# Kernel tuning notes

Hardware: AMD Instinct MI355X
Metric: run time of the kernel (lower is better)

## Reference

```python
import jax, jax.numpy as jnp
import numpy as np

B, S, E, H = 4, 2048, 256, 8
D = E // H
SCALE = D ** -0.5


def setup_inputs() -> dict:
    key = jax.random.key(0)
    k1, k2, k3, k4, k5, k6 = jax.random.split(key, 6)
    x = jax.random.normal(k1, (B, S, E), dtype=jnp.float32)
    lengths = jax.random.randint(k2, (B,), S // 4, S + 1)
    # binary prefix mask, as assumed by mask[i].sum() == valid length in the original
    mask = (jnp.arange(S)[None, :] < lengths[:, None]).astype(jnp.int32)
    w_std = 1.0 / np.sqrt(E)
    Wq = jax.random.normal(k3, (E, E), dtype=jnp.float32) * w_std
    Wk = jax.random.normal(k4, (E, E), dtype=jnp.float32) * w_std
    Wv = jax.random.normal(k5, (E, E), dtype=jnp.float32) * w_std
    Wo = jax.random.normal(k6, (E, E), dtype=jnp.float32) * w_std
    return {"x": x, "mask": mask, "Wq": Wq, "Wk": Wk, "Wv": Wv, "Wo": Wo}


def _scramble_pad(attn_i, L):
    # attn_i: [S, H, D] attention output for one sample; only query rows < L are used.
    # Faithful to torch: attn[:L] viewed as [H, L, D] (after transpose(1,2)) then
    # reshape(L, E), zero-padded to [S, E]. The reshape mixes heads in a
    # length-dependent way, reproduced here with integer index arithmetic.
    L_safe = jnp.maximum(L, 1)
    flat = jnp.arange(S * E)                     # flat index into [H, L, D] row-major
    h = jnp.minimum(flat // (L_safe * D), H - 1)
    rem = flat % (L_safe * D)
    s = rem // D
    d = rem % D
    valid = flat < L * E
    vals = attn_i[s, h, d]
    return jnp.where(valid, vals, 0.0).reshape(S, E)


def reference(x, mask, Wq, Wk, Wv, Wo):
    # projections (torch Linear, no bias: y = x @ W.T), split heads
    Q = (x @ Wq.T).reshape(B, S, H, D)
    K = (x @ Wk.T).reshape(B, S, H, D)
    V = (x @ Wv.T).reshape(B, S, H, D)
    scores = jnp.einsum("bqhd,bkhd->bhqk", Q, K) * SCALE
    key_valid = mask[:, None, None, :] > 0       # prefix key mask == per-sample varlen attn
    scores = jnp.where(key_valid, scores, -1e30)
    P = jax.nn.softmax(scores, axis=-1)
    attn = jnp.einsum("bhqk,bkhd->bqhd", P, V)   # [B, S, H, D]
    lengths = mask.sum(axis=1)
    padded = jax.vmap(_scramble_pad)(attn, lengths)  # [B, S, E]
    return padded @ Wo.T
```

## Files before the change

kernel.cpp:

```cpp
#include <hip/hip_runtime.h>
#include <cmath>

#define Bn 4
#define Sn 2048
#define En 256
#define Hn 8
#define Dn 32
#define KD 256
#define NS 4
#define CHUNK 512

static constexpr float SCALE_F = 0.17677669529663687f;
static constexpr float SCALE_LOG2E = 0.25504210472155044f;

typedef _Float16 half4_t __attribute__((ext_vector_type(4)));
typedef _Float16 half8_t __attribute__((ext_vector_type(8)));
typedef float float4_t __attribute__((ext_vector_type(4)));

__global__ __launch_bounds__(256) void cvt_kernel(
    const float* __restrict__ x, const float* __restrict__ Wq,
    const float* __restrict__ Wk, const float* __restrict__ Wv,
    const float* __restrict__ Wo, const int* __restrict__ mask,
    _Float16* __restrict__ xh, _Float16* __restrict__ Wh,
    int* __restrict__ len) {
  if (blockIdx.x == 1152) {
    const int b = threadIdx.x >> 6, lane = threadIdx.x & 63;
    int s = 0;
    for (int i = lane; i < Sn; i += 64) s += mask[b * Sn + i];
#pragma unroll
    for (int off = 32; off > 0; off >>= 1) s += __shfl_down(s, off, 64);
    if (lane == 0) len[b] = s;
    return;
  }
  const size_t base = ((size_t)blockIdx.x * 256 + threadIdx.x) * 8;
  const float* src; _Float16* dst; size_t off;
  if (base < 2097152) { src = x; dst = xh; off = base; }
  else {
    size_t wi = base - 2097152;
    int w = (int)(wi >> 16);
    off = wi & 65535;
    src = (w == 0) ? Wq : (w == 1) ? Wk : (w == 2) ? Wv : Wo;
    dst = Wh + (size_t)w * 65536;
  }
  float4 a = *(const float4*)&src[off];
  float4 b2 = *(const float4*)&src[off + 4];
  half8_t h;
  h[0] = (_Float16)a.x;  h[1] = (_Float16)a.y;
  h[2] = (_Float16)a.z;  h[3] = (_Float16)a.w;
  h[4] = (_Float16)b2.x; h[5] = (_Float16)b2.y;
  h[6] = (_Float16)b2.z; h[7] = (_Float16)b2.w;
  *(half8_t*)&dst[off] = h;
}

__global__ __launch_bounds__(256) void qkv_gemm(
    const _Float16* __restrict__ xh, const _Float16* __restrict__ Wh,
    _Float16* __restrict__ Qh, _Float16* __restrict__ Kh,
    _Float16* __restrict__ Vt) {
  const int lane = threadIdx.x & 63;
  const int wv = threadIdx.x >> 6;
  const int quad = lane >> 4, l15 = lane & 15;
  const int fid = blockIdx.x + 12 * blockIdx.y;
  const int wl = (fid & 7) * 48 + (fid >> 3);
  const int nb = wl % 12, mb = wl / 12;
  const int n0 = nb * 64;
  const int mw = mb * 256 + wv * 64;

  float4_t C[4][4];
#pragma unroll
  for (int i = 0; i < 4; ++i)
#pragma unroll
    for (int j = 0; j < 4; ++j) C[i][j] = (float4_t){0.f, 0.f, 0.f, 0.f};

  for (int k0 = 0; k0 < KD; k0 += 32) {
    half8_t A[4], Bf[4];
#pragma unroll
    for (int i = 0; i < 4; ++i)
      A[i] = *(const half8_t*)&xh[(size_t)(mw + 16 * i + l15) * KD + k0 + quad * 8];
#pragma unroll
    for (int j = 0; j < 4; ++j)
      Bf[j] = *(const half8_t*)&Wh[(size_t)(n0 + 16 * j + l15) * KD + k0 + quad * 8];
#pragma unroll
    for (int i = 0; i < 4; ++i)
#pragma unroll
      for (int j = 0; j < 4; ++j)
        C[i][j] = __builtin_amdgcn_mfma_f32_16x16x32_f16(A[i], Bf[j], C[i][j], 0, 0, 0);
  }

  const int mat = n0 >> 8;
  if (mat < 2) {
    _Float16* dstH = mat ? Kh : Qh;
    const float scale = mat ? 1.0f : SCALE_LOG2E;
#pragma unroll
    for (int i = 0; i < 4; ++i)
#pragma unroll
      for (int j = 0; j < 4; ++j) {
        const int c = ((n0 + 16 * j) & 255) + l15;
        const int h = c >> 5, d = c & 31;
#pragma unroll
        for (int r = 0; r < 4; ++r) {
          const int m = mw + 16 * i + quad * 4 + r;
          const int b = m >> 11, s = m & (Sn - 1);
          dstH[((size_t)(b * Hn + h) * Sn + s) * Dn + d] =
              (_Float16)(C[i][j][r] * scale);
        }
      }
  } else {
#pragma unroll
    for (int i = 0; i < 4; ++i)
#pragma unroll
      for (int j = 0; j < 4; ++j) {
        const int c = ((n0 + 16 * j) & 255) + l15;
        const int h = c >> 5, d = c & 31;
        const int m = mw + 16 * i + quad * 4;
        const int b = m >> 11, s = m & (Sn - 1);
        half4_t hv;
#pragma unroll
        for (int r = 0; r < 4; ++r) hv[r] = (_Float16)C[i][j][r];
        *(half4_t*)&Vt[(size_t)(b * Hn + h) * (Sn * Dn) +
                       (size_t)(s >> 5) * 1024 + d * 32 + (s & 31)] = hv;
      }
  }
}

__global__ __launch_bounds__(256) void out_gemm(
    const _Float16* __restrict__ Ph, const _Float16* __restrict__ Woh,
    float* __restrict__ out) {
  const int lane = threadIdx.x & 63;
  const int wv = threadIdx.x >> 6;
  const int quad = lane >> 4, l15 = lane & 15;
  const int fid = blockIdx.x + 4 * blockIdx.y;
  const int wl = (fid & 7) * 16 + (fid >> 3);
  const int nb = wl % 4, mb = wl / 4;
  const int n0 = nb * 64;
  const int mw = mb * 256 + wv * 64;

  float4_t C[4][4];
#pragma unroll
  for (int i = 0; i < 4; ++i)
#pragma unroll
    for (int j = 0; j < 4; ++j) C[i][j] = (float4_t){0.f, 0.f, 0.f, 0.f};

  for (int k0 = 0; k0 < KD; k0 += 32) {
    half8_t A[4], Bf[4];
#pragma unroll
    for (int i = 0; i < 4; ++i)
      A[i] = *(const half8_t*)&Ph[(size_t)(mw + 16 * i + l15) * KD + k0 + quad * 8];
#pragma unroll
    for (int j = 0; j < 4; ++j)
      Bf[j] = *(const half8_t*)&Woh[(size_t)(n0 + 16 * j + l15) * KD + k0 + quad * 8];
#pragma unroll
    for (int i = 0; i < 4; ++i)
#pragma unroll
      for (int j = 0; j < 4; ++j)
        C[i][j] = __builtin_amdgcn_mfma_f32_16x16x32_f16(A[i], Bf[j], C[i][j], 0, 0, 0);
  }

#pragma unroll
  for (int i = 0; i < 4; ++i)
#pragma unroll
    for (int j = 0; j < 4; ++j)
#pragma unroll
      for (int r = 0; r < 4; ++r)
        out[(size_t)(mw + 16 * i + quad * 4 + r) * En + n0 + 16 * j + l15] =
            C[i][j][r];
}

__global__ __launch_bounds__(256) void attn_kernel(
    const _Float16* __restrict__ Qh, const _Float16* __restrict__ Kh,
    const _Float16* __restrict__ Vt, const int* __restrict__ len,
    _Float16* __restrict__ pacc, float* __restrict__ pl) {
  const int lid = blockIdx.x + 32 * (blockIdx.y + 8 * blockIdx.z);
  const int h = lid & 7;
  const int w = lid >> 3;
  const int b = w >> 5;
  const int inner = w & 31;
  const int split = inner & (NS - 1);
  const int qg = inner >> 2;

  const int L = len[b];
  const int lane = threadIdx.x & 63;
  const int wv = threadIdx.x >> 6;
  const int q0 = (qg * 4 + wv) * 64;
  if (q0 >= L) return;
  const int ks = split * CHUNK;
  if (ks >= L) return;
  const int ke = min(L, ks + CHUNK);

  const int quad = lane >> 4;
  const int l15 = lane & 15;
  const size_t bh = (size_t)(b * Hn + h) * Sn;
  const _Float16* Vt0 = &Vt[(size_t)(b * Hn + h) * (Sn * Dn)];

  half8_t qf[4];
#pragma unroll
  for (int t = 0; t < 4; ++t)
    qf[t] = *(const half8_t*)&Qh[(bh + q0 + 16 * t + l15) * Dn + quad * 8];

  float4_t o0[4], o1[4];
  float ll[4];
#pragma unroll
  for (int t = 0; t < 4; ++t) {
    o0[t] = (float4_t){0.f, 0.f, 0.f, 0.f};
    o1[t] = (float4_t){0.f, 0.f, 0.f, 0.f};
    ll[t] = 0.f;
  }

  const int vo0 = l15 * 32 + quad * 4;
  const int vo1 = (l15 + 16) * 32 + quad * 4;

  const _Float16* vt_c = &Vt0[(size_t)(ks >> 5) * 1024];
  half8_t kfc0 = *(const half8_t*)&Kh[(bh + ks + l15) * Dn + quad * 8];
  half8_t kfc1 = *(const half8_t*)&Kh[(bh + ks + 16 + l15) * Dn + quad * 8];
  half4_t v0c = *(const half4_t*)&vt_c[vo0];
  half4_t v1c = *(const half4_t*)&vt_c[vo1];
  half4_t v2c = *(const half4_t*)&vt_c[vo0 + 16];
  half4_t v3c = *(const half4_t*)&vt_c[vo1 + 16];

  for (int k0 = ks; k0 < ke; k0 += 32) {
    const int kn = (k0 + 32 < ke) ? k0 + 32 : ks;
    const _Float16* vt_n = &Vt0[(size_t)(kn >> 5) * 1024];
    const half8_t kfn0 = *(const half8_t*)&Kh[(bh + kn + l15) * Dn + quad * 8];
    const half8_t kfn1 = *(const half8_t*)&Kh[(bh + kn + 16 + l15) * Dn + quad * 8];
    const half4_t v0n = *(const half4_t*)&vt_n[vo0];
    const half4_t v1n = *(const half4_t*)&vt_n[vo1];
    const half4_t v2n = *(const half4_t*)&vt_n[vo0 + 16];
    const half4_t v3n = *(const half4_t*)&vt_n[vo1 + 16];

    float4_t st0[4], st1[4];
#pragma unroll
    for (int t = 0; t < 4; ++t) {
      st0[t] = (float4_t){0.f, 0.f, 0.f, 0.f};
      st1[t] = (float4_t){0.f, 0.f, 0.f, 0.f};
      st0[t] = __builtin_amdgcn_mfma_f32_16x16x32_f16(kfc0, qf[t], st0[t], 0, 0, 0);
      st1[t] = __builtin_amdgcn_mfma_f32_16x16x32_f16(kfc1, qf[t], st1[t], 0, 0, 0);
    }

    if (k0 + 32 <= ke) {
#pragma unroll
      for (int t = 0; t < 4; ++t) {
        half4_t pf0, pf1;
#pragma unroll
        for (int r = 0; r < 4; ++r) {
          const float pa = __builtin_amdgcn_exp2f(st0[t][r]);
          const float pb = __builtin_amdgcn_exp2f(st1[t][r]);
          ll[t] += pa + pb;
          pf0[r] = (_Float16)pa;
          pf1[r] = (_Float16)pb;
        }
        o0[t] = __builtin_amdgcn_mfma_f32_16x16x16f16(pf0, v0c, o0[t], 0, 0, 0);
        o1[t] = __builtin_amdgcn_mfma_f32_16x16x16f16(pf0, v1c, o1[t], 0, 0, 0);
        o0[t] = __builtin_amdgcn_mfma_f32_16x16x16f16(pf1, v2c, o0[t], 0, 0, 0);
        o1[t] = __builtin_amdgcn_mfma_f32_16x16x16f16(pf1, v3c, o1[t], 0, 0, 0);
      }
    } else {
      const int ka = k0 + quad * 4, kb = k0 + 16 + quad * 4;
#pragma unroll
      for (int t = 0; t < 4; ++t) {
        half4_t pf0, pf1;
#pragma unroll
        for (int r = 0; r < 4; ++r) {
          const float pa = __builtin_amdgcn_exp2f((ka + r < ke) ? st0[t][r] : -3.0e38f);
          const float pb = __builtin_amdgcn_exp2f((kb + r < ke) ? st1[t][r] : -3.0e38f);
          ll[t] += pa + pb;
          pf0[r] = (_Float16)pa;
          pf1[r] = (_Float16)pb;
        }
        o0[t] = __builtin_amdgcn_mfma_f32_16x16x16f16(pf0, v0c, o0[t], 0, 0, 0);
        o1[t] = __builtin_amdgcn_mfma_f32_16x16x16f16(pf0, v1c, o1[t], 0, 0, 0);
        o0[t] = __builtin_amdgcn_mfma_f32_16x16x16f16(pf1, v2c, o0[t], 0, 0, 0);
        o1[t] = __builtin_amdgcn_mfma_f32_16x16x16f16(pf1, v3c, o1[t], 0, 0, 0);
      }
    }
    kfc0 = kfn0; kfc1 = kfn1;
    v0c = v0n; v1c = v1n; v2c = v2n; v3c = v3n;
  }

#pragma unroll
  for (int t = 0; t < 4; ++t) {
    ll[t] += __shfl_xor(ll[t], 16);
    ll[t] += __shfl_xor(ll[t], 32);
  }

  const size_t idx0 = ((size_t)(b * Hn + h) * NS + split) * Sn + q0;
#pragma unroll
  for (int t = 0; t < 4; ++t) {
#pragma unroll
    for (int r = 0; r < 4; ++r) {
      _Float16* pp = &pacc[(idx0 + 16 * t + quad * 4 + r) * 32];
      pp[l15] = (_Float16)o0[t][r];
      pp[l15 + 16] = (_Float16)o1[t][r];
    }
  }
  if (quad == 0) {
#pragma unroll
    for (int t = 0; t < 4; ++t) pl[idx0 + 16 * t + l15] = ll[t];
  }
}

__global__ __launch_bounds__(256) void combine_kernel(const _Float16* __restrict__ pacc,
                                                      const float* __restrict__ pl,
                                                      const int* __restrict__ len,
                                                      _Float16* __restrict__ Ph) {
  const int b = blockIdx.z;
  const int L = len[b];
  if (blockIdx.y == Hn) {
    _Float16* base = Ph + (size_t)b * Sn * En;
    const size_t end = (size_t)Sn * En;
    const size_t stride = (size_t)gridDim.x * 256 * 8;
    half8_t z = {0, 0, 0, 0, 0, 0, 0, 0};
    for (size_t idx = (size_t)L * En + ((size_t)blockIdx.x * 256 + threadIdx.x) * 8;
         idx < end; idx += stride)
      *(half8_t*)&base[idx] = z;
    return;
  }
  const int h = blockIdx.y;
  const int q = blockIdx.x * 256 + threadIdx.x;
  if (q >= L) return;
  const size_t base = (size_t)(b * Hn + h) * NS * Sn;

  float T = 0.f;
  float o[32];
#pragma unroll
  for (int d = 0; d < 32; ++d) o[d] = 0.f;
#pragma unroll
  for (int sp = 0; sp < NS; ++sp) {
    if (sp * CHUNK < L) {
      T += pl[base + (size_t)sp * Sn + q];
      const half8_t* pp = (const half8_t*)&pacc[(base + (size_t)sp * Sn + q) * 32];
#pragma unroll
      for (int i = 0; i < 4; ++i) {
        half8_t v = pp[i];
#pragma unroll
        for (int t2 = 0; t2 < 8; ++t2) o[i * 8 + t2] += (float)v[t2];
      }
    }
  }
  const float inv = 1.0f / T;
  _Float16* dst = &Ph[(size_t)b * Sn * En + (size_t)h * L * Dn + (size_t)q * Dn];
#pragma unroll
  for (int i = 0; i < 4; ++i) {
    half8_t hv;
#pragma unroll
    for (int t2 = 0; t2 < 8; ++t2) hv[t2] = (_Float16)(o[i * 8 + t2] * inv);
    *(half8_t*)&dst[i * 8] = hv;
  }
}

extern "C" void kernel_launch(void* const* d_in, const int* in_sizes, int n_in,
                              void* d_out, int out_size, void* d_ws, size_t ws_size,
                              hipStream_t stream) {
  (void)in_sizes; (void)n_in; (void)out_size; (void)ws_size;
  const float* x  = (const float*)d_in[0];
  const int* mask = (const int*)d_in[1];
  const float* Wq = (const float*)d_in[2];
  const float* Wk = (const float*)d_in[3];
  const float* Wv = (const float*)d_in[4];
  const float* Wo = (const float*)d_in[5];
  float* out = (float*)d_out;

  float* wsf = (float*)d_ws;
  int* lengths = (int*)d_ws;
  const size_t BHSD = (size_t)Bn * Hn * Sn * Dn;
  _Float16* xh = (_Float16*)(wsf + 64);
  _Float16* Wh = xh + BHSD;
  _Float16* Qh = Wh + 4 * 65536;
  _Float16* Kh = Qh + BHSD;
  _Float16* Vt = Kh + BHSD;
  _Float16* Ph = Vt + BHSD;
  _Float16* pacc = Ph + BHSD;
  float* pl = (float*)(pacc + (size_t)Bn * Hn * NS * Sn * 32);

  cvt_kernel<<<dim3((2097152 + 262144) / (256 * 8) + 1), 256, 0, stream>>>(
      x, Wq, Wk, Wv, Wo, mask, xh, Wh, lengths);
  qkv_gemm<<<dim3(12, 32), 256, 0, stream>>>(xh, Wh, Qh, Kh, Vt);
  attn_kernel<<<dim3((Sn / 256) * NS, Hn, Bn), 256, 0, stream>>>(
      Qh, Kh, Vt, lengths, pacc, pl);
  combine_kernel<<<dim3(Sn / 256, Hn + 1, Bn), 256, 0, stream>>>(
      pacc, pl, lengths, Ph);
  out_gemm<<<dim3(4, 32), 256, 0, stream>>>(Ph, Wh + 3 * 65536, out);
}
```

Measured before the change: 135.3 us.

## Fuse x fp16 conversion into QKV GEMM and halve attention query tile

Drops the separate x-to-fp16 pass: the QKV GEMM now reads fp32 x directly and converts in registers, so the conversion kernel only handles the weights and the mask lengths. This removes one full write and reread of x. The attention kernel now gives each wave 32 queries instead of 64, doubling the grid, which spreads work over more CUs and trims idle blocks past the valid length. The cost is that each block reuses its K/V loads over fewer queries, and the GEMM's A-operand loads double in bytes.

```diff
diff --git a/kernel.cpp b/kernel.cpp
--- a/kernel.cpp
+++ b/kernel.cpp
@@ -10,7 +10,6 @@
 #define NS 4
 #define CHUNK 512
 
-static constexpr float SCALE_F = 0.17677669529663687f;
 static constexpr float SCALE_LOG2E = 0.25504210472155044f;
 
 typedef _Float16 half4_t __attribute__((ext_vector_type(4)));
@@ -18,12 +17,11 @@
 typedef float float4_t __attribute__((ext_vector_type(4)));
 
 __global__ __launch_bounds__(256) void cvt_kernel(
-    const float* __restrict__ x, const float* __restrict__ Wq,
-    const float* __restrict__ Wk, const float* __restrict__ Wv,
-    const float* __restrict__ Wo, const int* __restrict__ mask,
-    _Float16* __restrict__ xh, _Float16* __restrict__ Wh,
+    const float* __restrict__ Wq, const float* __restrict__ Wk,
+    const float* __restrict__ Wv, const float* __restrict__ Wo,
+    const int* __restrict__ mask, _Float16* __restrict__ Wh,
     int* __restrict__ len) {
-  if (blockIdx.x == 1152) {
+  if (blockIdx.x == 128) {
     const int b = threadIdx.x >> 6, lane = threadIdx.x & 63;
     int s = 0;
     for (int i = lane; i < Sn; i += 64) s += mask[b * Sn + i];
@@ -32,16 +30,10 @@
     if (lane == 0) len[b] = s;
     return;
   }
-  const size_t base = ((size_t)blockIdx.x * 256 + threadIdx.x) * 8;
-  const float* src; _Float16* dst; size_t off;
-  if (base < 2097152) { src = x; dst = xh; off = base; }
-  else {
-    size_t wi = base - 2097152;
-    int w = (int)(wi >> 16);
-    off = wi & 65535;
-    src = (w == 0) ? Wq : (w == 1) ? Wk : (w == 2) ? Wv : Wo;
-    dst = Wh + (size_t)w * 65536;
-  }
+  const size_t wi = ((size_t)blockIdx.x * 256 + threadIdx.x) * 8;
+  const int w = (int)(wi >> 16);
+  const size_t off = wi & 65535;
+  const float* src = (w == 0) ? Wq : (w == 1) ? Wk : (w == 2) ? Wv : Wo;
   float4 a = *(const float4*)&src[off];
   float4 b2 = *(const float4*)&src[off + 4];
   half8_t h;
@@ -49,11 +41,11 @@
   h[2] = (_Float16)a.z;  h[3] = (_Float16)a.w;
   h[4] = (_Float16)b2.x; h[5] = (_Float16)b2.y;
   h[6] = (_Float16)b2.z; h[7] = (_Float16)b2.w;
-  *(half8_t*)&dst[off] = h;
+  *(half8_t*)&(Wh + (size_t)w * 65536)[off] = h;
 }
 
 __global__ __launch_bounds__(256) void qkv_gemm(
-    const _Float16* __restrict__ xh, const _Float16* __restrict__ Wh,
+    const float* __restrict__ x, const _Float16* __restrict__ Wh,
     _Float16* __restrict__ Qh, _Float16* __restrict__ Kh,
     _Float16* __restrict__ Vt) {
   const int lane = threadIdx.x & 63;
@@ -74,8 +66,15 @@
   for (int k0 = 0; k0 < KD; k0 += 32) {
     half8_t A[4], Bf[4];
 #pragma unroll
-    for (int i = 0; i < 4; ++i)
-      A[i] = *(const half8_t*)&xh[(size_t)(mw + 16 * i + l15) * KD + k0 + quad * 8];
+    for (int i = 0; i < 4; ++i) {
+      const float4* xp =
+          (const float4*)&x[(size_t)(mw + 16 * i + l15) * KD + k0 + quad * 8];
+      const float4 a0 = xp[0], a1 = xp[1];
+      A[i][0] = (_Float16)a0.x; A[i][1] = (_Float16)a0.y;
+      A[i][2] = (_Float16)a0.z; A[i][3] = (_Float16)a0.w;
+      A[i][4] = (_Float16)a1.x; A[i][5] = (_Float16)a1.y;
+      A[i][6] = (_Float16)a1.z; A[i][7] = (_Float16)a1.w;
+    }
 #pragma unroll
     for (int j = 0; j < 4; ++j)
       Bf[j] = *(const half8_t*)&Wh[(size_t)(n0 + 16 * j + l15) * KD + k0 + quad * 8];
@@ -169,18 +168,18 @@
     const _Float16* __restrict__ Qh, const _Float16* __restrict__ Kh,
     const _Float16* __restrict__ Vt, const int* __restrict__ len,
     _Float16* __restrict__ pacc, float* __restrict__ pl) {
-  const int lid = blockIdx.x + 32 * (blockIdx.y + 8 * blockIdx.z);
+  const int lid = blockIdx.x + 64 * (blockIdx.y + 8 * blockIdx.z);
   const int h = lid & 7;
-  const int w = lid >> 3;
-  const int b = w >> 5;
-  const int inner = w & 31;
+  const int rest = lid >> 3;
+  const int b = rest >> 6;
+  const int inner = rest & 63;
   const int split = inner & (NS - 1);
   const int qg = inner >> 2;
 
   const int L = len[b];
   const int lane = threadIdx.x & 63;
   const int wv = threadIdx.x >> 6;
-  const int q0 = (qg * 4 + wv) * 64;
+  const int q0 = (qg * 4 + wv) * 32;
   if (q0 >= L) return;
   const int ks = split * CHUNK;
   if (ks >= L) return;
@@ -191,15 +190,15 @@
   const size_t bh = (size_t)(b * Hn + h) * Sn;
   const _Float16* Vt0 = &Vt[(size_t)(b * Hn + h) * (Sn * Dn)];
 
-  half8_t qf[4];
-#pragma unroll
-  for (int t = 0; t < 4; ++t)
+  half8_t qf[2];
+#pragma unroll
+  for (int t = 0; t < 2; ++t)
     qf[t] = *(const half8_t*)&Qh[(bh + q0 + 16 * t + l15) * Dn + quad * 8];
 
-  float4_t o0[4], o1[4];
-  float ll[4];
-#pragma unroll
-  for (int t = 0; t < 4; ++t) {
+  float4_t o0[2], o1[2];
+  float ll[2];
+#pragma unroll
+  for (int t = 0; t < 2; ++t) {
     o0[t] = (float4_t){0.f, 0.f, 0.f, 0.f};
     o1[t] = (float4_t){0.f, 0.f, 0.f, 0.f};
     ll[t] = 0.f;
@@ -226,9 +225,9 @@
     const half4_t v2n = *(const half4_t*)&vt_n[vo0 + 16];
     const half4_t v3n = *(const half4_t*)&vt_n[vo1 + 16];
 
-    float4_t st0[4], st1[4];
-#pragma unroll
-    for (int t = 0; t < 4; ++t) {
+    float4_t st0[2], st1[2];
+#pragma unroll
+    for (int t = 0; t < 2; ++t) {
       st0[t] = (float4_t){0.f, 0.f, 0.f, 0.f};
       st1[t] = (float4_t){0.f, 0.f, 0.f, 0.f};
       st0[t] = __builtin_amdgcn_mfma_f32_16x16x32_f16(kfc0, qf[t], st0[t], 0, 0, 0);
@@ -237,7 +236,7 @@
 
     if (k0 + 32 <= ke) {
 #pragma unroll
-      for (int t = 0; t < 4; ++t) {
+      for (int t = 0; t < 2; ++t) {
         half4_t pf0, pf1;
 #pragma unroll
         for (int r = 0; r < 4; ++r) {
@@ -255,7 +254,7 @@
     } else {
       const int ka = k0 + quad * 4, kb = k0 + 16 + quad * 4;
 #pragma unroll
-      for (int t = 0; t < 4; ++t) {
+      for (int t = 0; t < 2; ++t) {
         half4_t pf0, pf1;
 #pragma unroll
         for (int r = 0; r < 4; ++r) {
@@ -276,14 +275,14 @@
   }
 
 #pragma unroll
-  for (int t = 0; t < 4; ++t) {
+  for (int t = 0; t < 2; ++t) {
     ll[t] += __shfl_xor(ll[t], 16);
     ll[t] += __shfl_xor(ll[t], 32);
   }
 
   const size_t idx0 = ((size_t)(b * Hn + h) * NS + split) * Sn + q0;
 #pragma unroll
-  for (int t = 0; t < 4; ++t) {
+  for (int t = 0; t < 2; ++t) {
 #pragma unroll
     for (int r = 0; r < 4; ++r) {
       _Float16* pp = &pacc[(idx0 + 16 * t + quad * 4 + r) * 32];
@@ -293,7 +292,7 @@
   }
   if (quad == 0) {
 #pragma unroll
-    for (int t = 0; t < 4; ++t) pl[idx0 + 16 * t + l15] = ll[t];
+    for (int t = 0; t < 2; ++t) pl[idx0 + 16 * t + l15] = ll[t];
   }
 }
 
@@ -361,8 +360,7 @@
   float* wsf = (float*)d_ws;
   int* lengths = (int*)d_ws;
   const size_t BHSD = (size_t)Bn * Hn * Sn * Dn;
-  _Float16* xh = (_Float16*)(wsf + 64);
-  _Float16* Wh = xh + BHSD;
+  _Float16* Wh = (_Float16*)(wsf + 64);
   _Float16* Qh = Wh + 4 * 65536;
   _Float16* Kh = Qh + BHSD;
   _Float16* Vt = Kh + BHSD;
@@ -370,10 +368,9 @@
   _Float16* pacc = Ph + BHSD;
   float* pl = (float*)(pacc + (size_t)Bn * Hn * NS * Sn * 32);
 
-  cvt_kernel<<<dim3((2097152 + 262144) / (256 * 8) + 1), 256, 0, stream>>>(
-      x, Wq, Wk, Wv, Wo, mask, xh, Wh, lengths);
-  qkv_gemm<<<dim3(12, 32), 256, 0, stream>>>(xh, Wh, Qh, Kh, Vt);
-  attn_kernel<<<dim3((Sn / 256) * NS, Hn, Bn), 256, 0, stream>>>(
+  cvt_kernel<<<dim3(129), 256, 0, stream>>>(Wq, Wk, Wv, Wo, mask, Wh, lengths);
+  qkv_gemm<<<dim3(12, 32), 256, 0, stream>>>(x, Wh, Qh, Kh, Vt);
+  attn_kernel<<<dim3((Sn / 128) * NS, Hn, Bn), 256, 0, stream>>>(
       Qh, Kh, Vt, lengths, pacc, pl);
   combine_kernel<<<dim3(Sn / 256, Hn + 1, Bn), 256, 0, stream>>>(
       pacc, pl, lengths, Ph);
```

Measured after the change: 148.6 us. +9.9%, slower.

## Fuse fp32-to-fp16 conversion into GEMMs and mask padded rows in out_gemm

Applied to the files above, without the earlier changes.

Removes the separate conversion kernel: qkv_gemm and out_gemm now load fp32 x and weights directly and convert to fp16 in registers, and the mask-length reduction moves into an extra block row of qkv_gemm. The zero-fill of padded rows in combine_kernel is dropped; out_gemm instead skips loading A rows at or beyond L and feeds zeros. out_gemm is retiled to 32 rows per wave with twice as many blocks. The aim is to save one launch plus the fp16 staging writes and reads, at the cost of twice the fp32 load bandwidth and redundant per-block conversions inside the GEMMs.

```diff
diff --git a/kernel.cpp b/kernel.cpp
--- a/kernel.cpp
+++ b/kernel.cpp
@@ -10,20 +10,20 @@
 #define NS 4
 #define CHUNK 512
 
-static constexpr float SCALE_F = 0.17677669529663687f;
 static constexpr float SCALE_LOG2E = 0.25504210472155044f;
 
 typedef _Float16 half4_t __attribute__((ext_vector_type(4)));
 typedef _Float16 half8_t __attribute__((ext_vector_type(8)));
 typedef float float4_t __attribute__((ext_vector_type(4)));
 
-__global__ __launch_bounds__(256) void cvt_kernel(
+__global__ __launch_bounds__(256) void qkv_gemm(
     const float* __restrict__ x, const float* __restrict__ Wq,
     const float* __restrict__ Wk, const float* __restrict__ Wv,
-    const float* __restrict__ Wo, const int* __restrict__ mask,
-    _Float16* __restrict__ xh, _Float16* __restrict__ Wh,
+    const int* __restrict__ mask, _Float16* __restrict__ Qh,
+    _Float16* __restrict__ Kh, _Float16* __restrict__ Vt,
     int* __restrict__ len) {
-  if (blockIdx.x == 1152) {
+  if (blockIdx.y == 32) {
+    if (blockIdx.x != 0) return;
     const int b = threadIdx.x >> 6, lane = threadIdx.x & 63;
     int s = 0;
     for (int i = lane; i < Sn; i += 64) s += mask[b * Sn + i];
@@ -32,30 +32,6 @@
     if (lane == 0) len[b] = s;
     return;
   }
-  const size_t base = ((size_t)blockIdx.x * 256 + threadIdx.x) * 8;
-  const float* src; _Float16* dst; size_t off;
-  if (base < 2097152) { src = x; dst = xh; off = base; }
-  else {
-    size_t wi = base - 2097152;
-    int w = (int)(wi >> 16);
-    off = wi & 65535;
-    src = (w == 0) ? Wq : (w == 1) ? Wk : (w == 2) ? Wv : Wo;
-    dst = Wh + (size_t)w * 65536;
-  }
-  float4 a = *(const float4*)&src[off];
-  float4 b2 = *(const float4*)&src[off + 4];
-  half8_t h;
-  h[0] = (_Float16)a.x;  h[1] = (_Float16)a.y;
-  h[2] = (_Float16)a.z;  h[3] = (_Float16)a.w;
-  h[4] = (_Float16)b2.x; h[5] = (_Float16)b2.y;
-  h[6] = (_Float16)b2.z; h[7] = (_Float16)b2.w;
-  *(half8_t*)&dst[off] = h;
-}
-
-__global__ __launch_bounds__(256) void qkv_gemm(
-    const _Float16* __restrict__ xh, const _Float16* __restrict__ Wh,
-    _Float16* __restrict__ Qh, _Float16* __restrict__ Kh,
-    _Float16* __restrict__ Vt) {
   const int lane = threadIdx.x & 63;
   const int wv = threadIdx.x >> 6;
   const int quad = lane >> 4, l15 = lane & 15;
@@ -65,6 +41,10 @@
   const int n0 = nb * 64;
   const int mw = mb * 256 + wv * 64;
 
+  const int mat = n0 >> 8;
+  const float* Wsel = (mat == 0) ? Wq : (mat == 1) ? Wk : Wv;
+  const int nr0 = n0 & 255;
+
   float4_t C[4][4];
 #pragma unroll
   for (int i = 0; i < 4; ++i)
@@ -74,11 +54,25 @@
   for (int k0 = 0; k0 < KD; k0 += 32) {
     half8_t A[4], Bf[4];
 #pragma unroll
-    for (int i = 0; i < 4; ++i)
-      A[i] = *(const half8_t*)&xh[(size_t)(mw + 16 * i + l15) * KD + k0 + quad * 8];
-#pragma unroll
-    for (int j = 0; j < 4; ++j)
-      Bf[j] = *(const half8_t*)&Wh[(size_t)(n0 + 16 * j + l15) * KD + k0 + quad * 8];
+    for (int i = 0; i < 4; ++i) {
+      const float4* xp =
+          (const float4*)&x[(size_t)(mw + 16 * i + l15) * KD + k0 + quad * 8];
+      const float4 a0 = xp[0], a1 = xp[1];
+      A[i][0] = (_Float16)a0.x; A[i][1] = (_Float16)a0.y;
+      A[i][2] = (_Float16)a0.z; A[i][3] = (_Float16)a0.w;
+      A[i][4] = (_Float16)a1.x; A[i][5] = (_Float16)a1.y;
+      A[i][6] = (_Float16)a1.z; A[i][7] = (_Float16)a1.w;
+    }
+#pragma unroll
+    for (int j = 0; j < 4; ++j) {
+      const float4* wp =
+          (const float4*)&Wsel[(size_t)(nr0 + 16 * j + l15) * KD + k0 + quad * 8];
+      const float4 b0 = wp[0], b1 = wp[1];
+      Bf[j][0] = (_Float16)b0.x; Bf[j][1] = (_Float16)b0.y;
+      Bf[j][2] = (_Float16)b0.z; Bf[j][3] = (_Float16)b0.w;
+      Bf[j][4] = (_Float16)b1.x; Bf[j][5] = (_Float16)b1.y;
+      Bf[j][6] = (_Float16)b1.z; Bf[j][7] = (_Float16)b1.w;
+    }
 #pragma unroll
     for (int i = 0; i < 4; ++i)
 #pragma unroll
@@ -86,7 +80,6 @@
         C[i][j] = __builtin_amdgcn_mfma_f32_16x16x32_f16(A[i], Bf[j], C[i][j], 0, 0, 0);
   }
 
-  const int mat = n0 >> 8;
   if (mat < 2) {
     _Float16* dstH = mat ? Kh : Qh;
     const float scale = mat ? 1.0f : SCALE_LOG2E;
@@ -94,7 +87,7 @@
     for (int i = 0; i < 4; ++i)
 #pragma unroll
       for (int j = 0; j < 4; ++j) {
-        const int c = ((n0 + 16 * j) & 255) + l15;
+        const int c = nr0 + 16 * j + l15;
         const int h = c >> 5, d = c & 31;
 #pragma unroll
         for (int r = 0; r < 4; ++r) {
@@ -109,7 +102,7 @@
     for (int i = 0; i < 4; ++i)
 #pragma unroll
       for (int j = 0; j < 4; ++j) {
-        const int c = ((n0 + 16 * j) & 255) + l15;
+        const int c = nr0 + 16 * j + l15;
         const int h = c >> 5, d = c & 31;
         const int m = mw + 16 * i + quad * 4;
         const int b = m >> 11, s = m & (Sn - 1);
@@ -123,45 +116,59 @@
 }
 
 __global__ __launch_bounds__(256) void out_gemm(
-    const _Float16* __restrict__ Ph, const _Float16* __restrict__ Woh,
-    float* __restrict__ out) {
+    const _Float16* __restrict__ Ph, const float* __restrict__ Wo,
+    const int* __restrict__ len, float* __restrict__ out) {
   const int lane = threadIdx.x & 63;
   const int wv = threadIdx.x >> 6;
   const int quad = lane >> 4, l15 = lane & 15;
   const int fid = blockIdx.x + 4 * blockIdx.y;
-  const int wl = (fid & 7) * 16 + (fid >> 3);
-  const int nb = wl % 4, mb = wl / 4;
+  const int wl = (fid & 7) * 32 + (fid >> 3);
+  const int nb = wl & 3, mbb = wl >> 2;
   const int n0 = nb * 64;
-  const int mw = mb * 256 + wv * 64;
-
-  float4_t C[4][4];
-#pragma unroll
-  for (int i = 0; i < 4; ++i)
+  const int rw = mbb * 128 + wv * 32;
+  const int b = rw >> 11;
+  const int L = len[b];
+
+  float4_t C[2][4];
+#pragma unroll
+  for (int i = 0; i < 2; ++i)
 #pragma unroll
     for (int j = 0; j < 4; ++j) C[i][j] = (float4_t){0.f, 0.f, 0.f, 0.f};
 
   for (int k0 = 0; k0 < KD; k0 += 32) {
-    half8_t A[4], Bf[4];
-#pragma unroll
-    for (int i = 0; i < 4; ++i)
-      A[i] = *(const half8_t*)&Ph[(size_t)(mw + 16 * i + l15) * KD + k0 + quad * 8];
-#pragma unroll
-    for (int j = 0; j < 4; ++j)
-      Bf[j] = *(const half8_t*)&Woh[(size_t)(n0 + 16 * j + l15) * KD + k0 + quad * 8];
-#pragma unroll
-    for (int i = 0; i < 4; ++i)
+    half8_t A[2], Bf[4];
+#pragma unroll
+    for (int i = 0; i < 2; ++i) {
+      const int s = (rw + 16 * i + l15) & (Sn - 1);
+      half8_t a = {0, 0, 0, 0, 0, 0, 0, 0};
+      if (s < L)
+        a = *(const half8_t*)&Ph[(size_t)(rw + 16 * i + l15) * KD + k0 + quad * 8];
+      A[i] = a;
+    }
+#pragma unroll
+    for (int j = 0; j < 4; ++j) {
+      const float4* wp =
+          (const float4*)&Wo[(size_t)(n0 + 16 * j + l15) * KD + k0 + quad * 8];
+      const float4 b0 = wp[0], b1 = wp[1];
+      Bf[j][0] = (_Float16)b0.x; Bf[j][1] = (_Float16)b0.y;
+      Bf[j][2] = (_Float16)b0.z; Bf[j][3] = (_Float16)b0.w;
+      Bf[j][4] = (_Float16)b1.x; Bf[j][5] = (_Float16)b1.y;
+      Bf[j][6] = (_Float16)b1.z; Bf[j][7] = (_Float16)b1.w;
+    }
+#pragma unroll
+    for (int i = 0; i < 2; ++i)
 #pragma unroll
       for (int j = 0; j < 4; ++j)
         C[i][j] = __builtin_amdgcn_mfma_f32_16x16x32_f16(A[i], Bf[j], C[i][j], 0, 0, 0);
   }
 
 #pragma unroll
-  for (int i = 0; i < 4; ++i)
+  for (int i = 0; i < 2; ++i)
 #pragma unroll
     for (int j = 0; j < 4; ++j)
 #pragma unroll
       for (int r = 0; r < 4; ++r)
-        out[(size_t)(mw + 16 * i + quad * 4 + r) * En + n0 + 16 * j + l15] =
+        out[(size_t)(rw + 16 * i + quad * 4 + r) * En + n0 + 16 * j + l15] =
             C[i][j][r];
 }
 
@@ -303,16 +310,6 @@
                                                       _Float16* __restrict__ Ph) {
   const int b = blockIdx.z;
   const int L = len[b];
-  if (blockIdx.y == Hn) {
-    _Float16* base = Ph + (size_t)b * Sn * En;
-    const size_t end = (size_t)Sn * En;
-    const size_t stride = (size_t)gridDim.x * 256 * 8;
-    half8_t z = {0, 0, 0, 0, 0, 0, 0, 0};
-    for (size_t idx = (size_t)L * En + ((size_t)blockIdx.x * 256 + threadIdx.x) * 8;
-         idx < end; idx += stride)
-      *(half8_t*)&base[idx] = z;
-    return;
-  }
   const int h = blockIdx.y;
   const int q = blockIdx.x * 256 + threadIdx.x;
   if (q >= L) return;
@@ -361,21 +358,18 @@
   float* wsf = (float*)d_ws;
   int* lengths = (int*)d_ws;
   const size_t BHSD = (size_t)Bn * Hn * Sn * Dn;
-  _Float16* xh = (_Float16*)(wsf + 64);
-  _Float16* Wh = xh + BHSD;
-  _Float16* Qh = Wh + 4 * 65536;
+  _Float16* Qh = (_Float16*)(wsf + 64);
   _Float16* Kh = Qh + BHSD;
   _Float16* Vt = Kh + BHSD;
   _Float16* Ph = Vt + BHSD;
   _Float16* pacc = Ph + BHSD;
   float* pl = (float*)(pacc + (size_t)Bn * Hn * NS * Sn * 32);
 
-  cvt_kernel<<<dim3((2097152 + 262144) / (256 * 8) + 1), 256, 0, stream>>>(
-      x, Wq, Wk, Wv, Wo, mask, xh, Wh, lengths);
-  qkv_gemm<<<dim3(12, 32), 256, 0, stream>>>(xh, Wh, Qh, Kh, Vt);
+  qkv_gemm<<<dim3(12, 33), 256, 0, stream>>>(x, Wq, Wk, Wv, mask, Qh, Kh, Vt,
+                                             lengths);
   attn_kernel<<<dim3((Sn / 256) * NS, Hn, Bn), 256, 0, stream>>>(
       Qh, Kh, Vt, lengths, pacc, pl);
-  combine_kernel<<<dim3(Sn / 256, Hn + 1, Bn), 256, 0, stream>>>(
+  combine_kernel<<<dim3(Sn / 256, Hn, Bn), 256, 0, stream>>>(
       pacc, pl, lengths, Ph);
-  out_gemm<<<dim3(4, 32), 256, 0, stream>>>(Ph, Wh + 3 * 65536, out);
-}
+  out_gemm<<<dim3(4, 64), 256, 0, stream>>>(Ph, Wo, lengths, out);
+}
```

Result: slower. 146.7 us (+8.5%).
